# Kernel tuning notes

Hardware: AMD Instinct MI355X
Metric: run time of the kernel (lower is better)

## Reference

```python
import jax, jax.numpy as jnp
import numpy as np

B, T, C = 2, 2048, 1024
H = 16
D = C // H  # head_size = 64
FF = 4 * C
EPS = 1e-5


def _layernorm(x, g, b):
    mu = jnp.mean(x, axis=-1, keepdims=True)
    var = jnp.var(x, axis=-1, keepdims=True)
    return (x - mu) * jax.lax.rsqrt(var + EPS) * g + b


def setup_inputs() -> dict:
    key = jax.random.key(0)
    ks = jax.random.split(key, 12)
    s_in = 1.0 / np.sqrt(C)
    s_ff = 1.0 / np.sqrt(FF)
    return {
        "x": jax.random.normal(ks[0], (B, T, C), jnp.float32),
        "Wq": jax.random.uniform(ks[1], (H, C, D), jnp.float32, -s_in, s_in),
        "Wk": jax.random.uniform(ks[2], (H, C, D), jnp.float32, -s_in, s_in),
        "Wv": jax.random.uniform(ks[3], (H, C, D), jnp.float32, -s_in, s_in),
        "Wo": jax.random.uniform(ks[4], (C, C), jnp.float32, -s_in, s_in),
        "bo": jax.random.uniform(ks[5], (C,), jnp.float32, -s_in, s_in),
        "W1": jax.random.uniform(ks[6], (C, FF), jnp.float32, -s_in, s_in),
        "b1": jax.random.uniform(ks[7], (FF,), jnp.float32, -s_in, s_in),
        "W2": jax.random.uniform(ks[8], (FF, C), jnp.float32, -s_ff, s_ff),
        "b2": jax.random.uniform(ks[9], (C,), jnp.float32, -s_ff, s_ff),
        "g1": jnp.ones((C,), jnp.float32),
        "be1": jnp.zeros((C,), jnp.float32),
        "g2": jnp.ones((C,), jnp.float32),
        "be2": jnp.zeros((C,), jnp.float32),
    }


def reference(x, Wq, Wk, Wv, Wo, bo, W1, b1, W2, b2, g1, be1, g2, be2):
    h = _layernorm(x, g1, be1)
    # per-head projections (no bias), vectorized over heads
    q = jnp.einsum("btc,hcd->bhtd", h, Wq)
    k = jnp.einsum("btc,hcd->bhtd", h, Wk)
    v = jnp.einsum("btc,hcd->bhtd", h, Wv)
    # NOTE: original scales by n_embd**-0.5 (C, not head_size) -- faithful
    scores = jnp.einsum("bhtd,bhsd->bhts", q, k) * (C ** -0.5)
    causal = jnp.tril(jnp.ones((T, T), bool))
    scores = jnp.where(causal, scores, -jnp.inf)
    att = jax.nn.softmax(scores, axis=-1)
    out = jnp.einsum("bhts,bhsd->bhtd", att, v)
    out = out.transpose(0, 2, 1, 3).reshape(B, T, C)  # concat heads
    x = out @ Wo + bo + x  # attn residual (dropout=0 -> identity)
    h2 = _layernorm(x, g2, be2)
    ff = jax.nn.relu(h2 @ W1 + b1) @ W2 + b2
    return x + ff
```

## Files before the change

kernel.cpp:

```cpp
#include <hip/hip_runtime.h>
#include <stdint.h>

typedef unsigned short ushort_t;
typedef __attribute__((ext_vector_type(8))) short bf16x8;
typedef __attribute__((ext_vector_type(4))) float f32x4;

__device__ __forceinline__ unsigned short f2b(float f) {
  unsigned u = __float_as_uint(f);
  u += 0x7fffu + ((u >> 16) & 1u);
  return (unsigned short)(u >> 16);
}

__device__ __forceinline__ void async16(const void* g, void* l) {
  __builtin_amdgcn_global_load_lds(
      (const __attribute__((address_space(1))) void*)g,
      (__attribute__((address_space(3))) void*)l, 16, 0, 0);
}

__global__ __launch_bounds__(256) void ln_kernel(
    const float* __restrict__ x, const float* __restrict__ g,
    const float* __restrict__ be, ushort_t* __restrict__ out) {
  const int C = 1024;
  int row = blockIdx.x;
  const float4* xr = (const float4*)(x + (size_t)row * C);
  int tid = threadIdx.x;
  float4 v = xr[tid];
  float s = v.x + v.y + v.z + v.w;
  float sq = v.x * v.x + v.y * v.y + v.z * v.z + v.w * v.w;
  #pragma unroll
  for (int off = 32; off > 0; off >>= 1) {
    s += __shfl_xor(s, off);
    sq += __shfl_xor(sq, off);
  }
  __shared__ float ss[4], ssq[4];
  int wv = tid >> 6;
  if ((tid & 63) == 0) { ss[wv] = s; ssq[wv] = sq; }
  __syncthreads();
  s = ss[0] + ss[1] + ss[2] + ss[3];
  sq = ssq[0] + ssq[1] + ssq[2] + ssq[3];
  float mu = s * (1.f / C);
  float var = sq * (1.f / C) - mu * mu;
  float rs = rsqrtf(var + 1e-5f);
  float4 gv = ((const float4*)g)[tid];
  float4 bv = ((const float4*)be)[tid];
  ushort4 o;
  o.x = f2b((v.x - mu) * rs * gv.x + bv.x);
  o.y = f2b((v.y - mu) * rs * gv.y + bv.y);
  o.z = f2b((v.z - mu) * rs * gv.z + bv.z);
  o.w = f2b((v.w - mu) * rs * gv.w + bv.w);
  ((ushort4*)(out + (size_t)row * C))[tid] = o;
}

__global__ __launch_bounds__(256) void reduce2_kernel(
    const float* __restrict__ p0, const float* __restrict__ p1,
    const float* __restrict__ bias, const float* __restrict__ resid,
    float* __restrict__ out) {
  int idx = blockIdx.x * 256 + threadIdx.x;
  float4 a = ((const float4*)p0)[idx];
  float4 b = ((const float4*)p1)[idx];
  float4 r = ((const float4*)resid)[idx];
  float4 bi = ((const float4*)bias)[idx & 255];
  float4 o;
  o.x = a.x + b.x + r.x + bi.x;
  o.y = a.y + b.y + r.y + bi.y;
  o.z = a.z + b.z + r.z + bi.z;
  o.w = a.w + b.w + r.w + bi.w;
  ((float4*)out)[idx] = o;
}

__global__ __launch_bounds__(256) void transpose_cast_kernel(
    const float* __restrict__ in, ushort_t* __restrict__ out, int R, int Cin) {
  __shared__ float tile[32][33];
  int bz = blockIdx.z;
  in += (size_t)bz * R * Cin;
  out += (size_t)bz * R * Cin;
  int c0 = blockIdx.x * 32, r0 = blockIdx.y * 32;
  int tx = threadIdx.x, ty = threadIdx.y;
  #pragma unroll
  for (int i = 0; i < 4; i++)
    tile[ty + 8 * i][tx] = in[(size_t)(r0 + ty + 8 * i) * Cin + c0 + tx];
  __syncthreads();
  #pragma unroll
  for (int i = 0; i < 4; i++)
    out[(size_t)(c0 + ty + 8 * i) * R + r0 + tx] = f2b(tile[tx][ty + 8 * i]);
}

__global__ __launch_bounds__(256) void transpose_v_kernel(
    const ushort_t* __restrict__ qkv, ushort_t* __restrict__ vt) {
  __shared__ ushort_t tile[32][33];
  int bh = blockIdx.z;
  int b = bh >> 4, h = bh & 15;
  int d0 = blockIdx.x * 32, t0 = blockIdx.y * 32;
  int tx = threadIdx.x, ty = threadIdx.y;
  #pragma unroll
  for (int i = 0; i < 4; i++)
    tile[ty + 8 * i][tx] =
        qkv[(size_t)(b * 2048 + t0 + ty + 8 * i) * 3072 + 2048 + h * 64 + d0 + tx];
  __syncthreads();
  #pragma unroll
  for (int i = 0; i < 4; i++)
    vt[(size_t)(bh * 64 + d0 + ty + 8 * i) * 2048 + t0 + tx] = tile[tx][ty + 8 * i];
}

template <int BN, int N, int K, int FLAGS, int SK>
__global__ __launch_bounds__(256, 3) void gemm_bt_kernel(
    const ushort_t* __restrict__ A, const ushort_t* __restrict__ Bt,
    const float* __restrict__ bias, const float* __restrict__ resid,
    void* __restrict__ outv, float* __restrict__ pp0, float* __restrict__ pp1) {
  constexpr int KS = K / SK;
  __shared__ ushort_t Als[2][128 * 32];
  __shared__ ushort_t Bls[2][128 * 32];
  int tid = threadIdx.x, w = tid >> 6, lane = tid & 63, quad = lane >> 4, l16 = lane & 15;
  int fid = blockIdx.x;
  int bn_low = (fid >> 3) & 7;
  int meta = (fid & 7) | ((fid >> 6) << 3);
  int bm = meta & 31;
  int high = meta >> 5;
  int bn, zz;
  if constexpr (SK > 1) { zz = high; bn = bn_low; }
  else { zz = 0; bn = bn_low + 8 * high; }
  int bn0 = bn * 128, bm0 = bm * 128;
  int koff = (SK > 1) ? zz * KS : 0;
  int wm = (w >> 1) * 64, wn = (w & 1) * 64;
  f32x4 acc[4][4];
  #pragma unroll
  for (int i = 0; i < 4; i++)
    #pragma unroll
    for (int j = 0; j < 4; j++) acc[i][j] = f32x4{0.f, 0.f, 0.f, 0.f};
  const ushort_t* Ag = A + (size_t)bm0 * K + koff;
  const ushort_t* Bg = Bt + (size_t)bn0 * K + koff;
  int lr = lane >> 2, lco = (lane & 3) * 8;
  auto stage = [&](int k0, int bi) {
    async16(Ag + (size_t)(w * 32 + lr) * K + k0 + lco, &Als[bi][w * 1024]);
    async16(Ag + (size_t)(w * 32 + 16 + lr) * K + k0 + lco, &Als[bi][w * 1024 + 512]);
    async16(Bg + (size_t)(w * 32 + lr) * K + k0 + lco, &Bls[bi][w * 1024]);
    async16(Bg + (size_t)(w * 32 + 16 + lr) * K + k0 + lco, &Bls[bi][w * 1024 + 512]);
  };
  stage(0, 0);
  int s = 0;
  for (int k0 = 0; k0 < KS; k0 += 32, s ^= 1) {
    __syncthreads();
    if (k0 + 32 < KS) stage(k0 + 32, s ^ 1);
    bf16x8 af[4], bf[4];
    #pragma unroll
    for (int i = 0; i < 4; i++)
      af[i] = *(const bf16x8*)&Als[s][(wm + i * 16 + l16) * 32 + quad * 8];
    #pragma unroll
    for (int j = 0; j < 4; j++)
      bf[j] = *(const bf16x8*)&Bls[s][(wn + j * 16 + l16) * 32 + quad * 8];
    #pragma unroll
    for (int i = 0; i < 4; i++)
      #pragma unroll
      for (int j = 0; j < 4; j++)
        acc[i][j] = __builtin_amdgcn_mfma_f32_16x16x32_bf16(af[i], bf[j], acc[i][j], 0, 0, 0);
  }
  float* pdst = nullptr;
  if constexpr (SK > 1) pdst = zz ? pp1 : pp0;
  #pragma unroll
  for (int i = 0; i < 4; i++)
    #pragma unroll
    for (int j = 0; j < 4; j++)
      #pragma unroll
      for (int r = 0; r < 4; r++) {
        int row = bm0 + wm + i * 16 + quad * 4 + r;
        int col = bn0 + wn + j * 16 + l16;
        float v = acc[i][j][r];
        if constexpr (SK > 1) {
          pdst[(size_t)row * N + col] = v;
        } else {
          if constexpr (FLAGS & 4) v += bias[col];
          if constexpr (FLAGS & 8) v += resid[(size_t)row * N + col];
          if constexpr (FLAGS & 1) v = fmaxf(v, 0.f);
          if constexpr ((FLAGS & 2) != 0)
            ((ushort_t*)outv)[(size_t)row * N + col] = f2b(v);
          else
            ((float*)outv)[(size_t)row * N + col] = v;
        }
      }
}

template <int N, int K, int FLAGS, int SK>
__global__ __launch_bounds__(256, 3) void gemm_bt64_kernel(
    const ushort_t* __restrict__ A, const ushort_t* __restrict__ Bt,
    const float* __restrict__ bias, const float* __restrict__ resid,
    void* __restrict__ outv, float* __restrict__ pp0, float* __restrict__ pp1) {
  constexpr int KS = K / SK;
  constexpr int NBM = 32;
  constexpr int NBN = N / 64;
  constexpr int NWG = NBM * NBN * SK;
  __shared__ ushort_t Als[2][128 * 32];
  __shared__ ushort_t Bls[2][64 * 32];
  int tid = threadIdx.x, w = tid >> 6, lane = tid & 63, quad = lane >> 4, l16 = lane & 15;
  int bid = blockIdx.x;
  int swz = (bid & 7) * (NWG / 8) + (bid >> 3);
  int z = 0;
  if constexpr (SK > 1) { z = swz / (NBM * NBN); swz -= z * (NBM * NBN); }
  int bm = swz / NBN, bn = swz - bm * NBN;
  int bm0 = bm * 128, bn0 = bn * 64;
  int koff = z * KS;
  int wm = (w >> 1) * 64, wn = (w & 1) * 32;
  f32x4 acc[4][2];
  #pragma unroll
  for (int i = 0; i < 4; i++)
    #pragma unroll
    for (int j = 0; j < 2; j++) acc[i][j] = f32x4{0.f, 0.f, 0.f, 0.f};
  const ushort_t* Ag = A + (size_t)bm0 * K + koff;
  const ushort_t* Bg = Bt + (size_t)bn0 * K + koff;
  int lr = lane >> 2, lco = (lane & 3) * 8;
  auto stage = [&](int k0, int bi) {
    async16(Ag + (size_t)(w * 32 + lr) * K + k0 + lco, &Als[bi][w * 1024]);
    async16(Ag + (size_t)(w * 32 + 16 + lr) * K + k0 + lco, &Als[bi][w * 1024 + 512]);
    async16(Bg + (size_t)(w * 16 + lr) * K + k0 + lco, &Bls[bi][w * 512]);
  };
  stage(0, 0);
  int s = 0;
  for (int k0 = 0; k0 < KS; k0 += 32, s ^= 1) {
    __syncthreads();
    if (k0 + 32 < KS) stage(k0 + 32, s ^ 1);
    bf16x8 af[4], bf[2];
    #pragma unroll
    for (int i = 0; i < 4; i++)
      af[i] = *(const bf16x8*)&Als[s][(wm + i * 16 + l16) * 32 + quad * 8];
    #pragma unroll
    for (int j = 0; j < 2; j++)
      bf[j] = *(const bf16x8*)&Bls[s][(wn + j * 16 + l16) * 32 + quad * 8];
    #pragma unroll
    for (int i = 0; i < 4; i++)
      #pragma unroll
      for (int j = 0; j < 2; j++)
        acc[i][j] = __builtin_amdgcn_mfma_f32_16x16x32_bf16(af[i], bf[j], acc[i][j], 0, 0, 0);
  }
  float* pdst = nullptr;
  if constexpr (SK > 1) pdst = z ? pp1 : pp0;
  #pragma unroll
  for (int i = 0; i < 4; i++)
    #pragma unroll
    for (int j = 0; j < 2; j++)
      #pragma unroll
      for (int r = 0; r < 4; r++) {
        int row = bm0 + wm + i * 16 + quad * 4 + r;
        int col = bn0 + wn + j * 16 + l16;
        float v = acc[i][j][r];
        if constexpr (SK > 1) {
          pdst[(size_t)row * N + col] = v;
        } else {
          if constexpr (FLAGS & 4) v += bias[col];
          if constexpr (FLAGS & 8) v += resid[(size_t)row * N + col];
          if constexpr (FLAGS & 1) v = fmaxf(v, 0.f);
          if constexpr ((FLAGS & 2) != 0)
            ((ushort_t*)outv)[(size_t)row * N + col] = f2b(v);
          else
            ((float*)outv)[(size_t)row * N + col] = v;
        }
      }
}

__global__ __launch_bounds__(256, 4) void attn_kernel(
    const ushort_t* __restrict__ qkv, const ushort_t* __restrict__ vt,
    ushort_t* __restrict__ out) {
  const int T = 2048, CC = 3072;
  __shared__ ushort_t Kls[2][2 * 64 * 32];
  __shared__ ushort_t Vls[2][2 * 64 * 32];
  int fid = blockIdx.x;
  int bh = (fid & 7) * 4 + ((fid >> 3) & 3);
  int qb = 31 - (fid >> 5);
  int b = bh >> 4, h = bh & 15;
  int q0 = qb * 64;
  int tid = threadIdx.x, w = tid >> 6, lane = tid & 63, quad = lane >> 4, l16 = lane & 15;
  int srow = w * 16 + (lane >> 2);
  int sco = (lane & 3) * 8;
  const ushort_t* kg = qkv + (size_t)(b * T + srow) * CC + 1024 + h * 64 + sco;
  const ushort_t* vg = vt + (size_t)(bh * 64 + srow) * T + sco;
  int q0s = q0 + w * 16;
  int trow = q0s + l16;
  const ushort_t* qp = qkv + (size_t)(b * T + trow) * CC + h * 64 + quad * 8;
  bf16x8 aq[2] = { *(const bf16x8*)qp, *(const bf16x8*)(qp + 32) };
  f32x4 O[4];
  #pragma unroll
  for (int i = 0; i < 4; i++) O[i] = f32x4{0.f, 0.f, 0.f, 0.f};
  float mrun = -1e30f, lrun = 0.f;
  const float ksc = 0.03125f * 1.44269504f;
  int src0 = (quad & 1) * 32 + l16;
  int src1 = src0 + 16;
  bool hiq = quad >= 2;
  auto stage = [&](int kb, int bi) {
    int s0 = kb * 64;
    async16(kg + (size_t)s0 * CC, &Kls[bi][w * 512]);
    async16(kg + (size_t)s0 * CC + 32, &Kls[bi][2048 + w * 512]);
    async16(vg + s0, &Vls[bi][w * 512]);
    async16(vg + s0 + 32, &Vls[bi][2048 + w * 512]);
  };
  stage(0, 0);
  for (int kb = 0; kb <= qb; kb++) {
    __syncthreads();
    if (kb < qb) stage(kb + 1, (kb + 1) & 1);
    int bi = kb & 1;
    int s0 = kb * 64;
    bf16x8 kfr[4][2], vfr[4][2];
    #pragma unroll
    for (int t = 0; t < 4; t++)
      #pragma unroll
      for (int ks = 0; ks < 2; ks++) {
        kfr[t][ks] = *(const bf16x8*)&Kls[bi][(ks * 64 + t * 16 + l16) * 32 + quad * 8];
        vfr[t][ks] = *(const bf16x8*)&Vls[bi][(ks * 64 + t * 16 + l16) * 32 + quad * 8];
      }
    f32x4 st[4];
    #pragma unroll
    for (int t = 0; t < 4; t++) {
      st[t] = f32x4{0.f, 0.f, 0.f, 0.f};
      #pragma unroll
      for (int ks = 0; ks < 2; ks++)
        st[t] = __builtin_amdgcn_mfma_f32_16x16x32_bf16(kfr[t][ks], aq[ks], st[t], 0, 0, 0);
    }
    float sv[4][4];
    float vmax = -1e30f;
    if (kb == qb) {
      #pragma unroll
      for (int t = 0; t < 4; t++)
        #pragma unroll
        for (int r = 0; r < 4; r++) {
          float sc = st[t][r] * ksc;
          int scol = s0 + t * 16 + quad * 4 + r;
          if (scol > trow) sc = -1e30f;
          sv[t][r] = sc;
          vmax = fmaxf(vmax, sc);
        }
    } else {
      #pragma unroll
      for (int t = 0; t < 4; t++)
        #pragma unroll
        for (int r = 0; r < 4; r++) {
          float sc = st[t][r] * ksc;
          sv[t][r] = sc;
          vmax = fmaxf(vmax, sc);
        }
    }
    vmax = fmaxf(vmax, __shfl_xor(vmax, 16));
    vmax = fmaxf(vmax, __shfl_xor(vmax, 32));
    float mnew = fmaxf(mrun, vmax);
    float alpha = __builtin_amdgcn_exp2f(mrun - mnew);
    mrun = mnew;
    float psum = 0.f;
    int pk[4][2];
    #pragma unroll
    for (int t = 0; t < 4; t++) {
      float p0 = __builtin_amdgcn_exp2f(sv[t][0] - mnew);
      float p1 = __builtin_amdgcn_exp2f(sv[t][1] - mnew);
      float p2 = __builtin_amdgcn_exp2f(sv[t][2] - mnew);
      float p3 = __builtin_amdgcn_exp2f(sv[t][3] - mnew);
      psum += (p0 + p1) + (p2 + p3);
      pk[t][0] = (int)((unsigned)f2b(p0) | ((unsigned)f2b(p1) << 16));
      pk[t][1] = (int)((unsigned)f2b(p2) | ((unsigned)f2b(p3) << 16));
    }
    psum += __shfl_xor(psum, 16);
    psum += __shfl_xor(psum, 32);
    lrun = lrun * alpha + psum;
    #pragma unroll
    for (int dt = 0; dt < 4; dt++) O[dt] *= alpha;
    #pragma unroll
    for (int g32 = 0; g32 < 2; g32++) {
      int t0 = 2 * g32, t1 = t0 + 1;
      int a0 = __shfl(pk[t0][0], src0), b0 = __shfl(pk[t1][0], src0);
      int a1 = __shfl(pk[t0][1], src0), b1 = __shfl(pk[t1][1], src0);
      int a2 = __shfl(pk[t0][0], src1), b2 = __shfl(pk[t1][0], src1);
      int a3 = __shfl(pk[t0][1], src1), b3 = __shfl(pk[t1][1], src1);
      union { int4 i; bf16x8 h; } u;
      u.i.x = hiq ? b0 : a0;
      u.i.y = hiq ? b1 : a1;
      u.i.z = hiq ? b2 : a2;
      u.i.w = hiq ? b3 : a3;
      #pragma unroll
      for (int dt = 0; dt < 4; dt++)
        O[dt] = __builtin_amdgcn_mfma_f32_16x16x32_bf16(vfr[dt][g32], u.h, O[dt], 0, 0, 0);
    }
  }
  float inv = 1.f / lrun;
  #pragma unroll
  for (int dt = 0; dt < 4; dt++) {
    ushort4 o;
    unsigned short* op = (unsigned short*)&o;
    #pragma unroll
    for (int r = 0; r < 4; r++) op[r] = f2b(O[dt][r] * inv);
    *(ushort4*)&out[(size_t)(b * T + trow) * 1024 + h * 64 + dt * 16 + quad * 4] = o;
  }
}

extern "C" void kernel_launch(void* const* d_in, const int* in_sizes, int n_in,
                              void* d_out, int out_size, void* d_ws, size_t ws_size,
                              hipStream_t stream) {
  const int B = 2, T = 2048, C = 1024, H = 16, D = 64, FF = 4096;
  const int M = B * T;
  const float* x   = (const float*)d_in[0];
  const float* Wq  = (const float*)d_in[1];
  const float* Wk  = (const float*)d_in[2];
  const float* Wv  = (const float*)d_in[3];
  const float* Wo  = (const float*)d_in[4];
  const float* bo  = (const float*)d_in[5];
  const float* W1  = (const float*)d_in[6];
  const float* b1  = (const float*)d_in[7];
  const float* W2  = (const float*)d_in[8];
  const float* b2  = (const float*)d_in[9];
  const float* g1  = (const float*)d_in[10];
  const float* be1 = (const float*)d_in[11];
  const float* g2  = (const float*)d_in[12];
  const float* be2 = (const float*)d_in[13];
  float* out = (float*)d_out;

  char* ws = (char*)d_ws;
  size_t off = 0;
  auto alloc = [&](size_t bytes) {
    void* p = ws + off;
    off += (bytes + 255) & ~(size_t)255;
    return p;
  };
  ushort_t* qkvt = (ushort_t*)alloc((size_t)3 * C * C * 2);
  ushort_t* wot  = (ushort_t*)alloc((size_t)C * C * 2);
  ushort_t* w1t  = (ushort_t*)alloc((size_t)FF * C * 2);
  ushort_t* w2t  = (ushort_t*)alloc((size_t)C * FF * 2);
  ushort_t* hbuf = (ushort_t*)alloc((size_t)M * C * 2);
  ushort_t* big  = (ushort_t*)alloc((size_t)M * FF * 2);
  ushort_t* vtb  = (ushort_t*)alloc((size_t)M * C * 2);
  ushort_t* aout = (ushort_t*)alloc((size_t)M * C * 2);
  float*    x2   = (float*)alloc((size_t)M * C * 4);
  float* pf0 = (float*)vtb;
  float* pf1 = (float*)qkvt;

  dim3 tb(32, 8);
  transpose_cast_kernel<<<dim3(D / 32, C / 32, H), tb, 0, stream>>>(Wq, qkvt, C, D);
  transpose_cast_kernel<<<dim3(D / 32, C / 32, H), tb, 0, stream>>>(Wk, qkvt + (size_t)C * C, C, D);
  transpose_cast_kernel<<<dim3(D / 32, C / 32, H), tb, 0, stream>>>(Wv, qkvt + (size_t)2 * C * C, C, D);
  transpose_cast_kernel<<<dim3(C / 32, C / 32, 1), tb, 0, stream>>>(Wo, wot, C, C);
  transpose_cast_kernel<<<dim3(FF / 32, C / 32, 1), tb, 0, stream>>>(W1, w1t, C, FF);
  transpose_cast_kernel<<<dim3(C / 32, FF / 32, 1), tb, 0, stream>>>(W2, w2t, FF, C);
  ln_kernel<<<M, 256, 0, stream>>>(x, g1, be1, hbuf);
  gemm_bt_kernel<24, 3072, 1024, 2, 1><<<768, 256, 0, stream>>>(
      hbuf, qkvt, nullptr, nullptr, big, nullptr, nullptr);
  transpose_v_kernel<<<dim3(2, T / 32, B * H), tb, 0, stream>>>(big, vtb);
  attn_kernel<<<1024, 256, 0, stream>>>(big, vtb, aout);
  gemm_bt64_kernel<1024, 1024, 4 | 8, 1><<<512, 256, 0, stream>>>(
      aout, wot, bo, x, x2, nullptr, nullptr);
  ln_kernel<<<M, 256, 0, stream>>>(x2, g2, be2, hbuf);
  gemm_bt_kernel<32, 4096, 1024, 1 | 2 | 4, 1><<<1024, 256, 0, stream>>>(
      hbuf, w1t, b1, nullptr, big, nullptr, nullptr);
  gemm_bt64_kernel<1024, 4096, 0, 2><<<1024, 256, 0, stream>>>(
      big, w2t, nullptr, nullptr, nullptr, pf0, pf1);
  reduce2_kernel<<<M * C / 1024, 256, 0, stream>>>(pf0, pf1, b2, x2, out);
}
```

Measured before the change: 357.1 us.

## Triple-buffer GEMM LDS pipeline and drop split-K for the FFN down projection

Both GEMM kernels move from double to triple-buffered LDS staging, with explicit vmcnt waits so two tiles stay in flight. The old __syncthreads is replaced by a raw s_barrier, and MFMA priority is raised during compute. The W2 GEMM no longer uses split-K plus a separate reduce kernel; it runs with SK=1 and fuses bias and residual into the epilogue. This removes the partial-sum traffic and one launch, but halves the workgroup count for that GEMM and raises LDS use per block, which may limit occupancy.

```diff
diff --git a/kernel.cpp b/kernel.cpp
--- a/kernel.cpp
+++ b/kernel.cpp
@@ -51,23 +51,6 @@
   ((ushort4*)(out + (size_t)row * C))[tid] = o;
 }
 
-__global__ __launch_bounds__(256) void reduce2_kernel(
-    const float* __restrict__ p0, const float* __restrict__ p1,
-    const float* __restrict__ bias, const float* __restrict__ resid,
-    float* __restrict__ out) {
-  int idx = blockIdx.x * 256 + threadIdx.x;
-  float4 a = ((const float4*)p0)[idx];
-  float4 b = ((const float4*)p1)[idx];
-  float4 r = ((const float4*)resid)[idx];
-  float4 bi = ((const float4*)bias)[idx & 255];
-  float4 o;
-  o.x = a.x + b.x + r.x + bi.x;
-  o.y = a.y + b.y + r.y + bi.y;
-  o.z = a.z + b.z + r.z + bi.z;
-  o.w = a.w + b.w + r.w + bi.w;
-  ((float4*)out)[idx] = o;
-}
-
 __global__ __launch_bounds__(256) void transpose_cast_kernel(
     const float* __restrict__ in, ushort_t* __restrict__ out, int R, int Cin) {
   __shared__ float tile[32][33];
@@ -108,8 +91,9 @@
     const float* __restrict__ bias, const float* __restrict__ resid,
     void* __restrict__ outv, float* __restrict__ pp0, float* __restrict__ pp1) {
   constexpr int KS = K / SK;
-  __shared__ ushort_t Als[2][128 * 32];
-  __shared__ ushort_t Bls[2][128 * 32];
+  constexpr int NT = KS / 32;
+  __shared__ ushort_t Als[3][128 * 32];
+  __shared__ ushort_t Bls[3][128 * 32];
   int tid = threadIdx.x, w = tid >> 6, lane = tid & 63, quad = lane >> 4, l16 = lane & 15;
   int fid = blockIdx.x;
   int bn_low = (fid >> 3) & 7;
@@ -137,22 +121,31 @@
     async16(Bg + (size_t)(w * 32 + 16 + lr) * K + k0 + lco, &Bls[bi][w * 1024 + 512]);
   };
   stage(0, 0);
-  int s = 0;
-  for (int k0 = 0; k0 < KS; k0 += 32, s ^= 1) {
-    __syncthreads();
-    if (k0 + 32 < KS) stage(k0 + 32, s ^ 1);
+  stage(32, 1);
+  int rb = 0, sb = 2;
+  for (int t = 0; t < NT; ++t) {
+    if (t < NT - 1) asm volatile("s_waitcnt vmcnt(4)" ::: "memory");
+    else            asm volatile("s_waitcnt vmcnt(0)" ::: "memory");
+    __builtin_amdgcn_s_barrier();
+    if (t + 2 < NT) stage((t + 2) * 32, sb);
     bf16x8 af[4], bf[4];
     #pragma unroll
     for (int i = 0; i < 4; i++)
-      af[i] = *(const bf16x8*)&Als[s][(wm + i * 16 + l16) * 32 + quad * 8];
+      af[i] = *(const bf16x8*)&Als[rb][(wm + i * 16 + l16) * 32 + quad * 8];
     #pragma unroll
     for (int j = 0; j < 4; j++)
-      bf[j] = *(const bf16x8*)&Bls[s][(wn + j * 16 + l16) * 32 + quad * 8];
+      bf[j] = *(const bf16x8*)&Bls[rb][(wn + j * 16 + l16) * 32 + quad * 8];
+    asm volatile("s_waitcnt lgkmcnt(0)" ::: "memory");
+    __builtin_amdgcn_sched_barrier(0);
+    __builtin_amdgcn_s_setprio(1);
     #pragma unroll
     for (int i = 0; i < 4; i++)
       #pragma unroll
       for (int j = 0; j < 4; j++)
         acc[i][j] = __builtin_amdgcn_mfma_f32_16x16x32_bf16(af[i], bf[j], acc[i][j], 0, 0, 0);
+    __builtin_amdgcn_s_setprio(0);
+    rb = rb == 2 ? 0 : rb + 1;
+    sb = sb == 2 ? 0 : sb + 1;
   }
   float* pdst = nullptr;
   if constexpr (SK > 1) pdst = zz ? pp1 : pp0;
@@ -185,11 +178,12 @@
     const float* __restrict__ bias, const float* __restrict__ resid,
     void* __restrict__ outv, float* __restrict__ pp0, float* __restrict__ pp1) {
   constexpr int KS = K / SK;
+  constexpr int NT = KS / 32;
   constexpr int NBM = 32;
   constexpr int NBN = N / 64;
   constexpr int NWG = NBM * NBN * SK;
-  __shared__ ushort_t Als[2][128 * 32];
-  __shared__ ushort_t Bls[2][64 * 32];
+  __shared__ ushort_t Als[3][128 * 32];
+  __shared__ ushort_t Bls[3][64 * 32];
   int tid = threadIdx.x, w = tid >> 6, lane = tid & 63, quad = lane >> 4, l16 = lane & 15;
   int bid = blockIdx.x;
   int swz = (bid & 7) * (NWG / 8) + (bid >> 3);
@@ -213,22 +207,31 @@
     async16(Bg + (size_t)(w * 16 + lr) * K + k0 + lco, &Bls[bi][w * 512]);
   };
   stage(0, 0);
-  int s = 0;
-  for (int k0 = 0; k0 < KS; k0 += 32, s ^= 1) {
-    __syncthreads();
-    if (k0 + 32 < KS) stage(k0 + 32, s ^ 1);
+  stage(32, 1);
+  int rb = 0, sb = 2;
+  for (int t = 0; t < NT; ++t) {
+    if (t < NT - 1) asm volatile("s_waitcnt vmcnt(3)" ::: "memory");
+    else            asm volatile("s_waitcnt vmcnt(0)" ::: "memory");
+    __builtin_amdgcn_s_barrier();
+    if (t + 2 < NT) stage((t + 2) * 32, sb);
     bf16x8 af[4], bf[2];
     #pragma unroll
     for (int i = 0; i < 4; i++)
-      af[i] = *(const bf16x8*)&Als[s][(wm + i * 16 + l16) * 32 + quad * 8];
+      af[i] = *(const bf16x8*)&Als[rb][(wm + i * 16 + l16) * 32 + quad * 8];
     #pragma unroll
     for (int j = 0; j < 2; j++)
-      bf[j] = *(const bf16x8*)&Bls[s][(wn + j * 16 + l16) * 32 + quad * 8];
+      bf[j] = *(const bf16x8*)&Bls[rb][(wn + j * 16 + l16) * 32 + quad * 8];
+    asm volatile("s_waitcnt lgkmcnt(0)" ::: "memory");
+    __builtin_amdgcn_sched_barrier(0);
+    __builtin_amdgcn_s_setprio(1);
     #pragma unroll
     for (int i = 0; i < 4; i++)
       #pragma unroll
       for (int j = 0; j < 2; j++)
         acc[i][j] = __builtin_amdgcn_mfma_f32_16x16x32_bf16(af[i], bf[j], acc[i][j], 0, 0, 0);
+    __builtin_amdgcn_s_setprio(0);
+    rb = rb == 2 ? 0 : rb + 1;
+    sb = sb == 2 ? 0 : sb + 1;
   }
   float* pdst = nullptr;
   if constexpr (SK > 1) pdst = z ? pp1 : pp0;
@@ -422,8 +425,6 @@
   ushort_t* vtb  = (ushort_t*)alloc((size_t)M * C * 2);
   ushort_t* aout = (ushort_t*)alloc((size_t)M * C * 2);
   float*    x2   = (float*)alloc((size_t)M * C * 4);
-  float* pf0 = (float*)vtb;
-  float* pf1 = (float*)qkvt;
 
   dim3 tb(32, 8);
   transpose_cast_kernel<<<dim3(D / 32, C / 32, H), tb, 0, stream>>>(Wq, qkvt, C, D);
@@ -442,7 +443,6 @@
   ln_kernel<<<M, 256, 0, stream>>>(x2, g2, be2, hbuf);
   gemm_bt_kernel<32, 4096, 1024, 1 | 2 | 4, 1><<<1024, 256, 0, stream>>>(
       hbuf, w1t, b1, nullptr, big, nullptr, nullptr);
-  gemm_bt64_kernel<1024, 4096, 0, 2><<<1024, 256, 0, stream>>>(
-      big, w2t, nullptr, nullptr, nullptr, pf0, pf1);
-  reduce2_kernel<<<M * C / 1024, 256, 0, stream>>>(pf0, pf1, b2, x2, out);
-}
+  gemm_bt64_kernel<1024, 4096, 4 | 8, 1><<<512, 256, 0, stream>>>(
+      big, w2t, b2, x2, out, nullptr, nullptr);
+}
```

Result: slower. 373.4 us (+4.6%).
